# Kernel optimization log

Hardware: AMD Instinct MI355X
Metric: run time of the kernel (lower is better)

## Reference

```python
import jax, jax.numpy as jnp
import numpy as np
from jax import lax

P = 128   # patch_size
S = 64    # stride
K = 31    # PSF kernel size
NZ = 15   # number of Zernike coefficients
HID = 64  # aberration MLP hidden width


def setup_inputs() -> dict:
    key = jax.random.key(0)
    ks = jax.random.split(key, 8)
    B, C, H, W = 8, 3, 512, 512
    x_hat = jax.random.uniform(ks[0], (B, C, H, W), dtype=jnp.float32)
    w1 = jax.random.normal(ks[1], (2, HID), dtype=jnp.float32) * 0.5
    b1 = jnp.zeros((HID,), jnp.float32)
    w2 = jax.random.normal(ks[2], (HID, HID), dtype=jnp.float32) * 0.125
    b2 = jnp.zeros((HID,), jnp.float32)
    w3 = jax.random.normal(ks[3], (HID, NZ), dtype=jnp.float32) * 0.1
    b3 = jnp.zeros((NZ,), jnp.float32)
    zernike_basis = jax.random.normal(ks[4], (NZ, K, K), dtype=jnp.float32) * 0.5
    return {"x_hat": x_hat, "w1": w1, "b1": b1, "w2": w2, "b2": b2,
            "w3": w3, "b3": b3, "zernike_basis": zernike_basis}


def _hann(n):
    # torch.hann_window (periodic=True): 0.5*(1 - cos(2*pi*k/n))
    return 0.5 - 0.5 * jnp.cos(2.0 * jnp.pi * jnp.arange(n, dtype=jnp.float32) / n)


def _psf_from_coeffs(coeffs, basis):
    # coeffs: [N, NZ], basis: [NZ, K, K] -> normalized PSFs [N, K, K]
    phase = jnp.einsum('nz,zhw->nhw', coeffs, basis)          # [N, K, K]
    g = jnp.linspace(-1.0, 1.0, K, dtype=jnp.float32)
    r2 = g[:, None] ** 2 + g[None, :] ** 2
    mask = (r2 <= 1.0).astype(jnp.float32)                    # circular pupil
    pupil = mask * jnp.exp(1j * phase.astype(jnp.complex64))
    field = jnp.fft.fftshift(jnp.fft.fft2(jnp.fft.ifftshift(pupil, axes=(-2, -1))), axes=(-2, -1))
    psf = jnp.abs(field) ** 2
    psf = psf / (jnp.sum(psf, axis=(-2, -1), keepdims=True) + 1e-12)
    return psf


def _forward(x_hat, w1, b1, w2, b2, w3, b3, basis):
    B, C, H, W = x_hat.shape
    pad_h = (S - (H - P) % S) % S
    pad_w = (S - (W - P) % S) % S
    x = jnp.pad(x_hat, ((0, 0), (0, 0), (0, pad_h), (0, pad_w)), mode='reflect') \
        if (pad_h or pad_w) else x_hat
    H_pad, W_pad = x.shape[2], x.shape[3]
    n_h = (H_pad - P) // S + 1
    n_w = (W_pad - P) // S + 1
    N = n_h * n_w

    # ---- unfold into overlapping patches: [B*N, C, P, P] ----
    r0 = jnp.arange(n_h) * S
    c0 = jnp.arange(n_w) * S
    ridx = r0[:, None] + jnp.arange(P)[None, :]               # [n_h, P]
    cidx = c0[:, None] + jnp.arange(P)[None, :]               # [n_w, P]
    patches = x[:, :, ridx[:, None, :, None], cidx[None, :, None, :]]  # [B,C,n_h,n_w,P,P]
    patches = patches.transpose(0, 2, 3, 1, 4, 5).reshape(B * N, C, P, P)

    # ---- per-patch normalized center coords in [-1, 1] ----
    y_norm = (r0.astype(jnp.float32) + P / 2.0) / H_pad * 2.0 - 1.0
    x_norm = (c0.astype(jnp.float32) + P / 2.0) / W_pad * 2.0 - 1.0
    gy, gx = jnp.meshgrid(y_norm, x_norm, indexing='ij')
    coords = jnp.stack([gy, gx], axis=-1).reshape(N, 2)       # [N, 2]
    coords = jnp.tile(coords, (B, 1))                         # [B*N, 2]

    # ---- aberration MLP -> Zernike coeffs -> PSF kernels ----
    h = jax.nn.relu(coords @ w1 + b1)
    h = jax.nn.relu(h @ w2 + b2)
    coeffs = h @ w3 + b3                                      # [B*N, NZ]
    psf = _psf_from_coeffs(coeffs, basis)                     # [B*N, K, K], C_k = 1
    kf = psf[:, ::-1, ::-1]                                   # flip -> true convolution

    # ---- spatially varying per-patch conv (C>1, C_k==1 broadcast branch) ----
    BN = B * N
    pad = K // 2
    xp = jnp.pad(patches, ((0, 0), (0, 0), (pad, pad), (pad, pad)))
    lhs = xp.reshape(1, BN * C, P + 2 * pad, P + 2 * pad)
    rhs = jnp.broadcast_to(kf[:, None, :, :], (BN, C, K, K)).reshape(BN * C, 1, K, K)
    y = lax.conv_general_dilated(lhs, rhs, (1, 1), 'VALID',
                                 dimension_numbers=('NCHW', 'OIHW', 'NCHW'),
                                 feature_group_count=BN * C)
    y_patches = y.reshape(BN, C, P, P)

    # ---- Hann window + overlap-add fold ----
    hann = _hann(P)
    window = hann[:, None] * hann[None, :]                    # [P, P]
    y_patches = y_patches * window[None, None]

    idx = (ridx[:, None, :, None] * W_pad + cidx[None, :, None, :]).reshape(-1)  # [N*P*P]
    vals = y_patches.reshape(B, N, C, P, P).transpose(0, 2, 1, 3, 4).reshape(B, C, -1)
    y_accum = jnp.zeros((B, C, H_pad * W_pad), jnp.float32).at[:, :, idx].add(vals)
    y_accum = y_accum.reshape(B, C, H_pad, W_pad)

    wvals = jnp.broadcast_to(window, (N, P, P)).reshape(-1)
    w_accum = jnp.zeros((H_pad * W_pad,), jnp.float32).at[idx].add(wvals)
    w_accum = w_accum.reshape(1, 1, H_pad, W_pad)

    y_hat = y_accum / (w_accum + 1e-8)
    return y_hat[:, :, :H, :W]


def reference(x_hat, w1, b1, w2, b2, w3, b3, zernike_basis):
    return _forward(x_hat, w1, b1, w2, b2, w3, b3, zernike_basis)
```

## Files before the change

kernel.cpp:

```cpp
#include <hip/hip_runtime.h>
#include <math.h>

#define B_ 8
#define C_ 3
#define HW_ 512
#define P_ 128
#define S_ 64
#define K_ 31
#define NZ_ 15
#define HID_ 64
#define NPOS_ 49
#define BN_ (B_*NPOS_)

#define LSTRIDE_ 192
#define LROWB_ 384
#define TROWS_ 96
#define FRAG_U32_ 256
#define NSTEP_ 16
#define BPOS_U32_ (NSTEP_ * 3 * FRAG_U32_)

typedef __attribute__((ext_vector_type(8))) short bf16x8;
typedef __attribute__((ext_vector_type(4))) float f32x4;

__device__ __forceinline__ float hann128(int p) {
    return 0.5f - 0.5f * cosf(6.283185307179586f * (float)p / 128.0f);
}

__device__ __forceinline__ unsigned int bf16_rne(float f) {
    union { float f; unsigned int u; } v; v.f = f;
    unsigned int r = v.u + 0x7fffu + ((v.u >> 16) & 1u);
    return r >> 16;
}

__device__ __forceinline__ float bf16_to_f(unsigned int bits16) {
    union { unsigned int u; float f; } v; v.u = bits16 << 16;
    return v.f;
}

__global__ __launch_bounds__(1024) void psf_kernel(
    const float* __restrict__ w1, const float* __restrict__ b1,
    const float* __restrict__ w2, const float* __restrict__ b2,
    const float* __restrict__ w3, const float* __restrict__ b3,
    const float* __restrict__ basis, unsigned int* __restrict__ bfrags)
{
    __shared__ float h1[HID_], h2[HID_], coef[NZ_];
    __shared__ float pupR[961], pupI[961], tR[961], tI[961];
    __shared__ float rootR[31], rootI[31];
    __shared__ float red[16];
    int n = blockIdx.x;
    int nh = n / 7, nw = n % 7;
    int tid = threadIdx.x;
    float cy = (float)(nh * S_ + P_ / 2) * (2.0f / (float)HW_) - 1.0f;
    float cx = (float)(nw * S_ + P_ / 2) * (2.0f / (float)HW_) - 1.0f;

    if (tid < HID_) h1[tid] = fmaxf(0.0f, cy * w1[tid] + cx * w1[HID_ + tid] + b1[tid]);
    if (tid < 31) {
        float ang = -6.283185307179586f * (float)tid / 31.0f;
        rootR[tid] = cosf(ang);
        rootI[tid] = sinf(ang);
    }
    __syncthreads();
    if (tid < HID_) {
        float s = b2[tid];
        for (int k = 0; k < HID_; ++k) s = fmaf(h1[k], w2[k * HID_ + tid], s);
        h2[tid] = fmaxf(0.0f, s);
    }
    __syncthreads();
    if (tid < NZ_) {
        float s = b3[tid];
        for (int k = 0; k < HID_; ++k) s = fmaf(h2[k], w3[k * NZ_ + tid], s);
        coef[tid] = s;
    }
    __syncthreads();

    for (int idx = tid; idx < 961; idx += 1024) {
        int h = idx / 31, w = idx % 31;
        float ph = 0.0f;
        for (int z = 0; z < NZ_; ++z) ph = fmaf(coef[z], basis[z * 961 + idx], ph);
        int dh = h - 15, dw = w - 15;
        bool m = (dh * dh + dw * dw) <= 225;
        float sv, cv;
        sincosf(ph, &sv, &cv);
        pupR[idx] = m ? cv : 0.0f;
        pupI[idx] = m ? sv : 0.0f;
    }
    __syncthreads();

    for (int idx = tid; idx < 961; idx += 1024) {
        int h = idx / 31, k = idx % 31;
        float ar = 0.0f, ai = 0.0f;
        for (int w = 0; w < 31; ++w) {
            int tt = (k * w) % 31;
            float cr = rootR[tt], ci = rootI[tt];
            float pr = pupR[h * 31 + w], pi = pupI[h * 31 + w];
            ar += pr * cr - pi * ci;
            ai += pr * ci + pi * cr;
        }
        tR[idx] = ar; tI[idx] = ai;
    }
    __syncthreads();

    float lsum = 0.0f;
    for (int idx = tid; idx < 961; idx += 1024) {
        int u = idx / 31, k = idx % 31;
        float gr = 0.0f, gi = 0.0f;
        for (int h = 0; h < 31; ++h) {
            int tt = (u * h) % 31;
            float cr = rootR[tt], ci = rootI[tt];
            float ar = tR[h * 31 + k], ai = tI[h * 31 + k];
            gr += ar * cr - ai * ci;
            gi += ar * ci + ai * cr;
        }
        float p = gr * gr + gi * gi;
        pupR[idx] = p;
        lsum += p;
    }
    float v = lsum;
    #pragma unroll
    for (int off = 32; off >= 1; off >>= 1) v += __shfl_xor(v, off, 64);
    if ((tid & 63) == 0) red[tid >> 6] = v;
    __syncthreads();
    if (tid == 0) {
        float s = 0.0f;
        #pragma unroll
        for (int i = 0; i < 16; ++i) s += red[i];
        red[0] = 1.0f / (s + 1e-12f);
    }
    __syncthreads();
    float inv = red[0];
    for (int idx = tid; idx < 961; idx += 1024) {
        int j = idx / 31, i = idx % 31;
        int u = (15 - j + 31) % 31, vv = (15 - i + 31) % 31;
        tI[idx] = pupR[u * 31 + vv] * inv;
    }
    __syncthreads();

    unsigned int* bf = bfrags + (size_t)n * BPOS_U32_;
    for (int w2 = tid; w2 < BPOS_U32_; w2 += 1024) {
        int jc = w2 >> 8;
        int s = jc / 3, c = jc % 3;
        int rem = w2 & 255;
        int l = rem >> 2, ew = rem & 3;
        int nn = l & 15, kg = l >> 4;
        unsigned int pack = 0;
        #pragma unroll
        for (int q = 0; q < 2; ++q) {
            int e = ew * 2 + q;
            int kk = kg * 8 + e;
            int jrow = 2 * s + (kk >> 4);
            int tap = 16 * c + (kk & 15) - nn;
            float vx = (jrow >= 1 && jrow <= 31 && tap >= 1 && tap <= 31)
                       ? tI[(jrow - 1) * 31 + (tap - 1)] : 0.0f;
            pack |= bf16_rne(vx) << (16 * q);
        }
        bf[w2] = pack;
    }
}

template<int MODE>
__global__ __launch_bounds__(512, 4) void conv_mfma_kernel(
    const float* __restrict__ x, const unsigned int* __restrict__ bfrags,
    void* __restrict__ dst)
{
    __shared__ unsigned short sIn[TROWS_ * LSTRIDE_];
    __shared__ float sH[128];

    int t = blockIdx.x;
    int half = t & 1;
    int cc = (t >> 1) % 3;
    int bn = t / 6;
    int b = bn / NPOS_, n = bn % NPOS_;
    int nh = n / 7, nw = n % 7;
    int r0 = nh * S_, c0 = nw * S_;
    int tid = threadIdx.x;

    if (tid < 128) sH[tid] = hann128(tid);

    for (int i = tid; i < TROWS_ * LROWB_ / 16; i += 512)
        ((uint4*)sIn)[i] = make_uint4(0u, 0u, 0u, 0u);
    __syncthreads();

    const float* xb = x + ((size_t)(b * C_ + cc) * HW_ + r0) * HW_ + c0;
    int rpbase = half * 64 - 16;
    for (int i = tid; i < TROWS_ * 16; i += 512) {
        int r = i >> 4, c8 = (i & 15) * 8;
        int rp = rpbase + r;
        if (rp >= 0 && rp < P_) {
            float4 v0 = *(const float4*)&xb[rp * HW_ + c8];
            float4 v1 = *(const float4*)&xb[rp * HW_ + c8 + 4];
            uint4 o;
            o.x = bf16_rne(v0.x) | (bf16_rne(v0.y) << 16);
            o.y = bf16_rne(v0.z) | (bf16_rne(v0.w) << 16);
            o.z = bf16_rne(v1.x) | (bf16_rne(v1.y) << 16);
            o.w = bf16_rne(v1.z) | (bf16_rne(v1.w) << 16);
            int byteoff = (r * LROWB_ + 32 + c8 * 2) ^ ((r & 7) << 4);
            *(uint4*)((char*)sIn + byteoff) = o;
        }
    }
    __syncthreads();

    int lane = tid & 63, wv = tid >> 6;
    int m0 = (wv & 3) * 16;
    int ch = (wv >> 2) * 64;
    int lrow = lane & 15, lkg = lane >> 4;

    f32x4 acc[4];
    #pragma unroll
    for (int q = 0; q < 4; ++q) acc[q] = (f32x4){0.f, 0.f, 0.f, 0.f};

    int rowb = m0 + lrow + (lkg >> 1);
    int colb = ch * 2 + (lkg & 1) * 16;
    int xr[4];
    #pragma unroll
    for (int sm = 0; sm < 4; ++sm) xr[sm] = ((rowb + 2 * sm) & 7) << 4;
    const bf16x8* bpos = (const bf16x8*)(bfrags + (size_t)n * BPOS_U32_) + lane;

    bf16x8 A0[6], A1[6], B0[3], B1[3];

#define LOADA(DST, S) { int base_ = (rowb + 2 * (S)) * LROWB_ + colb; int x_ = xr[(S) & 3]; \
    _Pragma("unroll") for (int p_ = 0; p_ < 6; ++p_) \
        DST[p_] = *(const bf16x8*)((const char*)sIn + ((base_ + p_ * 32) ^ x_)); }
#define LOADB(DST, S) { const bf16x8* bp_ = bpos + (S) * 192; \
    DST[0] = bp_[0]; DST[1] = bp_[64]; DST[2] = bp_[128]; }
#define DOMFMA(AA, BB) { _Pragma("unroll") for (int q_ = 0; q_ < 4; ++q_) { \
    acc[q_] = __builtin_amdgcn_mfma_f32_16x16x32_bf16(AA[q_],     BB[0], acc[q_], 0, 0, 0); \
    acc[q_] = __builtin_amdgcn_mfma_f32_16x16x32_bf16(AA[q_ + 1], BB[1], acc[q_], 0, 0, 0); \
    acc[q_] = __builtin_amdgcn_mfma_f32_16x16x32_bf16(AA[q_ + 2], BB[2], acc[q_], 0, 0, 0); } }

    LOADA(A0, 0); LOADB(B0, 0);

    #pragma unroll
    for (int s2 = 0; s2 < 8; ++s2) {
        LOADA(A1, 2 * s2 + 1); LOADB(B1, 2 * s2 + 1);
        __builtin_amdgcn_sched_barrier(0);
        __builtin_amdgcn_s_setprio(1);
        DOMFMA(A0, B0);
        __builtin_amdgcn_s_setprio(0);
        __builtin_amdgcn_sched_barrier(0);
        if (s2 < 7) { LOADA(A0, 2 * s2 + 2); LOADB(B0, 2 * s2 + 2); }
        __builtin_amdgcn_sched_barrier(0);
        __builtin_amdgcn_s_setprio(1);
        DOMFMA(A1, B1);
        __builtin_amdgcn_s_setprio(0);
        __builtin_amdgcn_sched_barrier(0);
    }
#undef LOADA
#undef LOADB
#undef DOMFMA

    int prow0 = half * 64 + m0 + lkg * 4;
    float hy[4];
    #pragma unroll
    for (int r = 0; r < 4; ++r) hy[r] = sH[prow0 + r];

    #pragma unroll
    for (int q = 0; q < 4; ++q) {
        int pcol = ch + 16 * q + lrow;
        float hxv = sH[pcol];
        #pragma unroll
        for (int r = 0; r < 4; ++r) {
            int prow = prow0 + r;
            float val = acc[q][r] * hy[r] * hxv;
            if (MODE == 0) {
                unsigned short* yp = (unsigned short*)dst + (((size_t)bn * C_ + cc) << 14);
                yp[prow * P_ + pcol] = (unsigned short)bf16_rne(val);
            } else {
                float* ob = (float*)dst;
                atomicAdd(ob + ((size_t)(b * C_ + cc) * HW_ + r0 + prow) * HW_ + c0 + pcol, val);
            }
        }
    }
}

__global__ __launch_bounds__(256) void gather_kernel(
    const unsigned short* __restrict__ ypatch, float* __restrict__ out)
{
    __shared__ float sH[128];
    int tid = threadIdx.x;
    if (tid < 128) sH[tid] = hann128(tid);
    __syncthreads();

    int gid = blockIdx.x * 256 + tid;
    int base = gid * 4;
    if (base >= B_ * C_ * HW_ * HW_) return;
    int X = base & 511;
    int Y = (base >> 9) & 511;
    int bc = base >> 18;
    int c = bc % 3, b = bc / 3;
    int nhA = Y >> 6, pyA = Y & 63;
    int nwA = X >> 6, pxA = X & 63;
    bool vA = nhA <= 6, vB = nhA >= 1;
    bool uA = nwA <= 6, uB = nwA >= 1;
    float wy = (vA ? sH[pyA] : 0.0f) + (vB ? sH[pyA + 64] : 0.0f);

    float4 acc = {0.f, 0.f, 0.f, 0.f};
    #pragma unroll
    for (int sy = 0; sy < 2; ++sy) {
        bool okY = sy == 0 ? vA : vB;
        int nh = sy == 0 ? nhA : nhA - 1;
        int py = sy == 0 ? pyA : pyA + 64;
        #pragma unroll
        for (int sx = 0; sx < 2; ++sx) {
            bool okX = sx == 0 ? uA : uB;
            int nw = sx == 0 ? nwA : nwA - 1;
            int px = sx == 0 ? pxA : pxA + 64;
            if (okY && okX) {
                size_t off = ((((size_t)b * NPOS_ + nh * 7 + nw) * C_ + c) << 14) + (py << 7) + px;
                uint2 v = *(const uint2*)&ypatch[off];
                acc.x += bf16_to_f(v.x & 0xffffu);
                acc.y += bf16_to_f(v.x >> 16);
                acc.z += bf16_to_f(v.y & 0xffffu);
                acc.w += bf16_to_f(v.y >> 16);
            }
        }
    }
    float4 o;
    float wx0 = (uA ? sH[pxA + 0] : 0.0f) + (uB ? sH[pxA + 64] : 0.0f);
    float wx1 = (uA ? sH[pxA + 1] : 0.0f) + (uB ? sH[pxA + 65] : 0.0f);
    float wx2 = (uA ? sH[pxA + 2] : 0.0f) + (uB ? sH[pxA + 66] : 0.0f);
    float wx3 = (uA ? sH[pxA + 3] : 0.0f) + (uB ? sH[pxA + 67] : 0.0f);
    o.x = acc.x / (wy * wx0 + 1e-8f);
    o.y = acc.y / (wy * wx1 + 1e-8f);
    o.z = acc.z / (wy * wx2 + 1e-8f);
    o.w = acc.w / (wy * wx3 + 1e-8f);
    *(float4*)&out[base] = o;
}

__global__ __launch_bounds__(256) void divide_kernel(float* __restrict__ out)
{
    int idx = blockIdx.x * 256 + threadIdx.x;
    if (idx >= B_ * C_ * HW_ * HW_) return;
    int X = idx & 511;
    int Y = (idx >> 9) & 511;
    int nhA = Y >> 6, pyA = Y & 63;
    int nwA = X >> 6, pxA = X & 63;
    float wy = (nhA <= 6 ? hann128(pyA) : 0.0f) + (nhA >= 1 ? hann128(pyA + 64) : 0.0f);
    float wx = (nwA <= 6 ? hann128(pxA) : 0.0f) + (nwA >= 1 ? hann128(pxA + 64) : 0.0f);
    out[idx] = out[idx] / (wy * wx + 1e-8f);
}

extern "C" void kernel_launch(void* const* d_in, const int* in_sizes, int n_in,
                              void* d_out, int out_size, void* d_ws, size_t ws_size,
                              hipStream_t stream)
{
    const float* x    = (const float*)d_in[0];
    const float* w1   = (const float*)d_in[1];
    const float* b1   = (const float*)d_in[2];
    const float* w2   = (const float*)d_in[3];
    const float* b2   = (const float*)d_in[4];
    const float* w3   = (const float*)d_in[5];
    const float* b3   = (const float*)d_in[6];
    const float* basis = (const float*)d_in[7];
    float* out = (float*)d_out;

    unsigned int* bfrags = (unsigned int*)d_ws;
    size_t bfBytes = (size_t)NPOS_ * BPOS_U32_ * sizeof(unsigned int);
    size_t need = bfBytes + (size_t)BN_ * C_ * P_ * P_ * sizeof(unsigned short);

    psf_kernel<<<NPOS_, 1024, 0, stream>>>(w1, b1, w2, b2, w3, b3, basis, bfrags);

    int nPix = B_ * C_ * HW_ * HW_;
    if (ws_size >= need) {
        unsigned short* ypatch = (unsigned short*)((char*)d_ws + bfBytes);
        conv_mfma_kernel<0><<<BN_ * C_ * 2, 512, 0, stream>>>(x, bfrags, ypatch);
        gather_kernel<<<(nPix / 4 + 255) / 256, 256, 0, stream>>>(ypatch, out);
    } else {
        hipMemsetAsync(d_out, 0, (size_t)out_size * sizeof(float), stream);
        conv_mfma_kernel<1><<<BN_ * C_ * 2, 512, 0, stream>>>(x, bfrags, out);
        divide_kernel<<<(nPix + 255) / 256, 256, 0, stream>>>(out);
    }
}
```

Baseline: 80.83 us.

## Process full patch per block with 16x128 wave tiles and staggered step order

Each block now handles a whole 128x128 patch instead of half, so the input tile is loaded once into a 160-row LDS buffer rather than twice with halo overlap. Each wave computes a 16x128 output strip (8 accumulators), which lets A fragments be reused across more columns. Each wave also starts its K-step loop at a different offset, which spreads out LDS and global B-fragment accesses. The explicit double-buffered A pipeline with sched barriers is replaced by single-buffered A loads plus B prefetch. In exchange the grid is halved, LDS use rises, and register pressure grows from the larger accumulator and A arrays, which may reduce occupancy and latency hiding.

```diff
diff --git a/kernel.cpp b/kernel.cpp
--- a/kernel.cpp
+++ b/kernel.cpp
@@ -12,9 +12,8 @@
 #define NPOS_ 49
 #define BN_ (B_*NPOS_)
 
-#define LSTRIDE_ 192
 #define LROWB_ 384
-#define TROWS_ 96
+#define TROWS_ 160
 #define FRAG_U32_ 256
 #define NSTEP_ 16
 #define BPOS_U32_ (NSTEP_ * 3 * FRAG_U32_)
@@ -162,13 +161,12 @@
     const float* __restrict__ x, const unsigned int* __restrict__ bfrags,
     void* __restrict__ dst)
 {
-    __shared__ unsigned short sIn[TROWS_ * LSTRIDE_];
+    __shared__ unsigned short sIn[TROWS_ * (LROWB_ / 2)];
     __shared__ float sH[128];
 
     int t = blockIdx.x;
-    int half = t & 1;
-    int cc = (t >> 1) % 3;
-    int bn = t / 6;
+    int cc = t % 3;
+    int bn = t / 3;
     int b = bn / NPOS_, n = bn % NPOS_;
     int nh = n / 7, nw = n % 7;
     int r0 = nh * S_, c0 = nw * S_;
@@ -181,81 +179,74 @@
     __syncthreads();
 
     const float* xb = x + ((size_t)(b * C_ + cc) * HW_ + r0) * HW_ + c0;
-    int rpbase = half * 64 - 16;
-    for (int i = tid; i < TROWS_ * 16; i += 512) {
-        int r = i >> 4, c8 = (i & 15) * 8;
-        int rp = rpbase + r;
-        if (rp >= 0 && rp < P_) {
-            float4 v0 = *(const float4*)&xb[rp * HW_ + c8];
-            float4 v1 = *(const float4*)&xb[rp * HW_ + c8 + 4];
-            uint4 o;
-            o.x = bf16_rne(v0.x) | (bf16_rne(v0.y) << 16);
-            o.y = bf16_rne(v0.z) | (bf16_rne(v0.w) << 16);
-            o.z = bf16_rne(v1.x) | (bf16_rne(v1.y) << 16);
-            o.w = bf16_rne(v1.z) | (bf16_rne(v1.w) << 16);
-            int byteoff = (r * LROWB_ + 32 + c8 * 2) ^ ((r & 7) << 4);
-            *(uint4*)((char*)sIn + byteoff) = o;
-        }
+    for (int i = tid; i < 128 * 16; i += 512) {
+        int r = 16 + (i >> 4), c8 = (i & 15) * 8;
+        const float* rp = &xb[(r - 16) * HW_ + c8];
+        float4 v0 = *(const float4*)rp;
+        float4 v1 = *(const float4*)(rp + 4);
+        uint4 o;
+        o.x = bf16_rne(v0.x) | (bf16_rne(v0.y) << 16);
+        o.y = bf16_rne(v0.z) | (bf16_rne(v0.w) << 16);
+        o.z = bf16_rne(v1.x) | (bf16_rne(v1.y) << 16);
+        o.w = bf16_rne(v1.z) | (bf16_rne(v1.w) << 16);
+        int byteoff = (r * LROWB_ + 32 + c8 * 2) ^ ((r & 7) << 4);
+        *(uint4*)((char*)sIn + byteoff) = o;
     }
     __syncthreads();
 
     int lane = tid & 63, wv = tid >> 6;
-    int m0 = (wv & 3) * 16;
-    int ch = (wv >> 2) * 64;
+    int m0 = wv * 16;
     int lrow = lane & 15, lkg = lane >> 4;
 
-    f32x4 acc[4];
-    #pragma unroll
-    for (int q = 0; q < 4; ++q) acc[q] = (f32x4){0.f, 0.f, 0.f, 0.f};
+    f32x4 acc[8];
+    #pragma unroll
+    for (int q = 0; q < 8; ++q) acc[q] = (f32x4){0.f, 0.f, 0.f, 0.f};
 
     int rowb = m0 + lrow + (lkg >> 1);
-    int colb = ch * 2 + (lkg & 1) * 16;
-    int xr[4];
-    #pragma unroll
-    for (int sm = 0; sm < 4; ++sm) xr[sm] = ((rowb + 2 * sm) & 7) << 4;
+    int colb = (lkg & 1) * 16;
     const bf16x8* bpos = (const bf16x8*)(bfrags + (size_t)n * BPOS_U32_) + lane;
-
-    bf16x8 A0[6], A1[6], B0[3], B1[3];
-
-#define LOADA(DST, S) { int base_ = (rowb + 2 * (S)) * LROWB_ + colb; int x_ = xr[(S) & 3]; \
-    _Pragma("unroll") for (int p_ = 0; p_ < 6; ++p_) \
-        DST[p_] = *(const bf16x8*)((const char*)sIn + ((base_ + p_ * 32) ^ x_)); }
-#define LOADB(DST, S) { const bf16x8* bp_ = bpos + (S) * 192; \
-    DST[0] = bp_[0]; DST[1] = bp_[64]; DST[2] = bp_[128]; }
-#define DOMFMA(AA, BB) { _Pragma("unroll") for (int q_ = 0; q_ < 4; ++q_) { \
-    acc[q_] = __builtin_amdgcn_mfma_f32_16x16x32_bf16(AA[q_],     BB[0], acc[q_], 0, 0, 0); \
-    acc[q_] = __builtin_amdgcn_mfma_f32_16x16x32_bf16(AA[q_ + 1], BB[1], acc[q_], 0, 0, 0); \
-    acc[q_] = __builtin_amdgcn_mfma_f32_16x16x32_bf16(AA[q_ + 2], BB[2], acc[q_], 0, 0, 0); } }
-
-    LOADA(A0, 0); LOADB(B0, 0);
-
-    #pragma unroll
-    for (int s2 = 0; s2 < 8; ++s2) {
-        LOADA(A1, 2 * s2 + 1); LOADB(B1, 2 * s2 + 1);
-        __builtin_amdgcn_sched_barrier(0);
+    int sbase = wv * 2;
+
+    int ss0 = sbase & 15;
+    bf16x8 Bc0 = bpos[ss0 * 192], Bc1 = bpos[ss0 * 192 + 64], Bc2 = bpos[ss0 * 192 + 128];
+
+    #pragma unroll 2
+    for (int s = 0; s < NSTEP_; ++s) {
+        int ss = (s + sbase) & 15;
+        bf16x8 Bn0, Bn1, Bn2;
+        if (s + 1 < NSTEP_) {
+            int ssn = (s + 1 + sbase) & 15;
+            const bf16x8* bp = bpos + ssn * 192;
+            Bn0 = bp[0]; Bn1 = bp[64]; Bn2 = bp[128];
+        } else { Bn0 = Bc0; Bn1 = Bc1; Bn2 = Bc2; }
+
+        int r2 = rowb + 2 * ss;
+        int base = r2 * LROWB_ + colb;
+        int xorv = (r2 & 7) << 4;
+        bf16x8 A[10];
+        #pragma unroll
+        for (int p = 0; p < 10; ++p)
+            A[p] = *(const bf16x8*)((const char*)sIn + ((base + p * 32) ^ xorv));
+
         __builtin_amdgcn_s_setprio(1);
-        DOMFMA(A0, B0);
+        #pragma unroll
+        for (int q = 0; q < 8; ++q) {
+            acc[q] = __builtin_amdgcn_mfma_f32_16x16x32_bf16(A[q],     Bc0, acc[q], 0, 0, 0);
+            acc[q] = __builtin_amdgcn_mfma_f32_16x16x32_bf16(A[q + 1], Bc1, acc[q], 0, 0, 0);
+            acc[q] = __builtin_amdgcn_mfma_f32_16x16x32_bf16(A[q + 2], Bc2, acc[q], 0, 0, 0);
+        }
         __builtin_amdgcn_s_setprio(0);
-        __builtin_amdgcn_sched_barrier(0);
-        if (s2 < 7) { LOADA(A0, 2 * s2 + 2); LOADB(B0, 2 * s2 + 2); }
-        __builtin_amdgcn_sched_barrier(0);
-        __builtin_amdgcn_s_setprio(1);
-        DOMFMA(A1, B1);
-        __builtin_amdgcn_s_setprio(0);
-        __builtin_amdgcn_sched_barrier(0);
-    }
-#undef LOADA
-#undef LOADB
-#undef DOMFMA
-
-    int prow0 = half * 64 + m0 + lkg * 4;
+        Bc0 = Bn0; Bc1 = Bn1; Bc2 = Bn2;
+    }
+
+    int prow0 = m0 + lkg * 4;
     float hy[4];
     #pragma unroll
     for (int r = 0; r < 4; ++r) hy[r] = sH[prow0 + r];
 
     #pragma unroll
-    for (int q = 0; q < 4; ++q) {
-        int pcol = ch + 16 * q + lrow;
+    for (int q = 0; q < 8; ++q) {
+        int pcol = 16 * q + lrow;
         float hxv = sH[pcol];
         #pragma unroll
         for (int r = 0; r < 4; ++r) {
@@ -362,11 +353,11 @@
     int nPix = B_ * C_ * HW_ * HW_;
     if (ws_size >= need) {
         unsigned short* ypatch = (unsigned short*)((char*)d_ws + bfBytes);
-        conv_mfma_kernel<0><<<BN_ * C_ * 2, 512, 0, stream>>>(x, bfrags, ypatch);
+        conv_mfma_kernel<0><<<BN_ * C_, 512, 0, stream>>>(x, bfrags, ypatch);
         gather_kernel<<<(nPix / 4 + 255) / 256, 256, 0, stream>>>(ypatch, out);
     } else {
         hipMemsetAsync(d_out, 0, (size_t)out_size * sizeof(float), stream);
-        conv_mfma_kernel<1><<<BN_ * C_ * 2, 512, 0, stream>>>(x, bfrags, out);
+        conv_mfma_kernel<1><<<BN_ * C_, 512, 0, stream>>>(x, bfrags, out);
         divide_kernel<<<(nPix + 255) / 256, 256, 0, stream>>>(out);
     }
 }
```

Result: faster. 77.52 us (-4.1%).

## Widen per-wave conv tile to full 128 columns with inline-asm pipelined loads

Applied to the files above, without the earlier changes.

The conv block shrinks from 512 to 256 threads, and each wave now computes a 16x128 output strip with 8 accumulators instead of 16x64. A fragments loaded from LDS are then reused across twice as many MFMAs, and each B fragment is loaded once per wave instead of by two waves. LDS and global loads are issued through inline asm with explicit partial waitcnts, and each wave starts at a staggered k-step to spread bank and cache traffic. The cost is more registers per thread, a lower occupancy hint, and manual waitcnt counting that must match the number of loads in flight.

```diff
diff --git a/kernel.cpp b/kernel.cpp
--- a/kernel.cpp
+++ b/kernel.cpp
@@ -12,7 +12,6 @@
 #define NPOS_ 49
 #define BN_ (B_*NPOS_)
 
-#define LSTRIDE_ 192
 #define LROWB_ 384
 #define TROWS_ 96
 #define FRAG_U32_ 256
@@ -158,11 +157,11 @@
 }
 
 template<int MODE>
-__global__ __launch_bounds__(512, 4) void conv_mfma_kernel(
+__global__ __launch_bounds__(256, 3) void conv_mfma_kernel(
     const float* __restrict__ x, const unsigned int* __restrict__ bfrags,
     void* __restrict__ dst)
 {
-    __shared__ unsigned short sIn[TROWS_ * LSTRIDE_];
+    __shared__ unsigned short sIn[TROWS_ * (LROWB_ / 2)];
     __shared__ float sH[128];
 
     int t = blockIdx.x;
@@ -176,13 +175,13 @@
 
     if (tid < 128) sH[tid] = hann128(tid);
 
-    for (int i = tid; i < TROWS_ * LROWB_ / 16; i += 512)
+    for (int i = tid; i < TROWS_ * LROWB_ / 16; i += 256)
         ((uint4*)sIn)[i] = make_uint4(0u, 0u, 0u, 0u);
     __syncthreads();
 
     const float* xb = x + ((size_t)(b * C_ + cc) * HW_ + r0) * HW_ + c0;
     int rpbase = half * 64 - 16;
-    for (int i = tid; i < TROWS_ * 16; i += 512) {
+    for (int i = tid; i < TROWS_ * 16; i += 256) {
         int r = i >> 4, c8 = (i & 15) * 8;
         int rp = rpbase + r;
         if (rp >= 0 && rp < P_) {
@@ -200,52 +199,72 @@
     __syncthreads();
 
     int lane = tid & 63, wv = tid >> 6;
-    int m0 = (wv & 3) * 16;
-    int ch = (wv >> 2) * 64;
+    int m0 = wv * 16;
     int lrow = lane & 15, lkg = lane >> 4;
 
-    f32x4 acc[4];
-    #pragma unroll
-    for (int q = 0; q < 4; ++q) acc[q] = (f32x4){0.f, 0.f, 0.f, 0.f};
+    f32x4 acc[8];
+    #pragma unroll
+    for (int q = 0; q < 8; ++q) acc[q] = (f32x4){0.f, 0.f, 0.f, 0.f};
 
     int rowb = m0 + lrow + (lkg >> 1);
-    int colb = ch * 2 + (lkg & 1) * 16;
-    int xr[4];
-    #pragma unroll
-    for (int sm = 0; sm < 4; ++sm) xr[sm] = ((rowb + 2 * sm) & 7) << 4;
+    int colb = (lkg & 1) * 16;
+    unsigned lbase = (unsigned)(unsigned long long)(const void*)sIn;
     const bf16x8* bpos = (const bf16x8*)(bfrags + (size_t)n * BPOS_U32_) + lane;
-
-    bf16x8 A0[6], A1[6], B0[3], B1[3];
-
-#define LOADA(DST, S) { int base_ = (rowb + 2 * (S)) * LROWB_ + colb; int x_ = xr[(S) & 3]; \
-    _Pragma("unroll") for (int p_ = 0; p_ < 6; ++p_) \
-        DST[p_] = *(const bf16x8*)((const char*)sIn + ((base_ + p_ * 32) ^ x_)); }
-#define LOADB(DST, S) { const bf16x8* bp_ = bpos + (S) * 192; \
-    DST[0] = bp_[0]; DST[1] = bp_[64]; DST[2] = bp_[128]; }
-#define DOMFMA(AA, BB) { _Pragma("unroll") for (int q_ = 0; q_ < 4; ++q_) { \
+    int sbase = wv * 4;
+
+    bf16x8 A0[10], A1[10], B0[3], B1[3];
+
+#define ISSUE_A(DST, SS_) { \
+    int r2_ = rowb + 2 * (SS_); \
+    unsigned ro_ = (unsigned)(r2_ * LROWB_ + colb); \
+    unsigned xv_ = (unsigned)((r2_ & 7) << 4); \
+    _Pragma("unroll") \
+    for (int p_ = 0; p_ < 10; ++p_) { \
+        unsigned a_ = lbase + ((ro_ + (unsigned)(p_ * 32)) ^ xv_); \
+        asm volatile("ds_read_b128 %0, %1" : "=v"(DST[p_]) : "v"(a_)); \
+    } }
+
+#define ISSUE_B(DST, SS_) { \
+    const char* bp_ = (const char*)(bpos + (SS_) * 192); \
+    asm volatile("global_load_dwordx4 %0, %1, off"             : "=v"(DST[0]) : "v"(bp_)); \
+    asm volatile("global_load_dwordx4 %0, %1, off offset:1024" : "=v"(DST[1]) : "v"(bp_)); \
+    asm volatile("global_load_dwordx4 %0, %1, off offset:2048" : "=v"(DST[2]) : "v"(bp_)); }
+
+#define DOMFMA(AA, BB) { _Pragma("unroll") for (int q_ = 0; q_ < 8; ++q_) { \
     acc[q_] = __builtin_amdgcn_mfma_f32_16x16x32_bf16(AA[q_],     BB[0], acc[q_], 0, 0, 0); \
     acc[q_] = __builtin_amdgcn_mfma_f32_16x16x32_bf16(AA[q_ + 1], BB[1], acc[q_], 0, 0, 0); \
     acc[q_] = __builtin_amdgcn_mfma_f32_16x16x32_bf16(AA[q_ + 2], BB[2], acc[q_], 0, 0, 0); } }
 
-    LOADA(A0, 0); LOADB(B0, 0);
+    {
+        int ss0 = sbase & 15;
+        ISSUE_A(A0, ss0); ISSUE_B(B0, ss0);
+    }
 
     #pragma unroll
     for (int s2 = 0; s2 < 8; ++s2) {
-        LOADA(A1, 2 * s2 + 1); LOADB(B1, 2 * s2 + 1);
+        int se = (2 * s2 + 1 + sbase) & 15;
+        ISSUE_A(A1, se); ISSUE_B(B1, se);
+        asm volatile("s_waitcnt lgkmcnt(10) vmcnt(3)");
         __builtin_amdgcn_sched_barrier(0);
         __builtin_amdgcn_s_setprio(1);
         DOMFMA(A0, B0);
         __builtin_amdgcn_s_setprio(0);
         __builtin_amdgcn_sched_barrier(0);
-        if (s2 < 7) { LOADA(A0, 2 * s2 + 2); LOADB(B0, 2 * s2 + 2); }
+        if (s2 < 7) {
+            int so = (2 * s2 + 2 + sbase) & 15;
+            ISSUE_A(A0, so); ISSUE_B(B0, so);
+            asm volatile("s_waitcnt lgkmcnt(10) vmcnt(3)");
+        } else {
+            asm volatile("s_waitcnt lgkmcnt(0) vmcnt(0)");
+        }
         __builtin_amdgcn_sched_barrier(0);
         __builtin_amdgcn_s_setprio(1);
         DOMFMA(A1, B1);
         __builtin_amdgcn_s_setprio(0);
         __builtin_amdgcn_sched_barrier(0);
     }
-#undef LOADA
-#undef LOADB
+#undef ISSUE_A
+#undef ISSUE_B
 #undef DOMFMA
 
     int prow0 = half * 64 + m0 + lkg * 4;
@@ -254,8 +273,8 @@
     for (int r = 0; r < 4; ++r) hy[r] = sH[prow0 + r];
 
     #pragma unroll
-    for (int q = 0; q < 4; ++q) {
-        int pcol = ch + 16 * q + lrow;
+    for (int q = 0; q < 8; ++q) {
+        int pcol = 16 * q + lrow;
         float hxv = sH[pcol];
         #pragma unroll
         for (int r = 0; r < 4; ++r) {
@@ -362,11 +381,11 @@
     int nPix = B_ * C_ * HW_ * HW_;
     if (ws_size >= need) {
         unsigned short* ypatch = (unsigned short*)((char*)d_ws + bfBytes);
-        conv_mfma_kernel<0><<<BN_ * C_ * 2, 512, 0, stream>>>(x, bfrags, ypatch);
+        conv_mfma_kernel<0><<<BN_ * C_ * 2, 256, 0, stream>>>(x, bfrags, ypatch);
         gather_kernel<<<(nPix / 4 + 255) / 256, 256, 0, stream>>>(ypatch, out);
     } else {
         hipMemsetAsync(d_out, 0, (size_t)out_size * sizeof(float), stream);
-        conv_mfma_kernel<1><<<BN_ * C_ * 2, 512, 0, stream>>>(x, bfrags, out);
+        conv_mfma_kernel<1><<<BN_ * C_ * 2, 256, 0, stream>>>(x, bfrags, out);
         divide_kernel<<<(nPix + 255) / 256, 256, 0, stream>>>(out);
     }
 }
```

Result: faster. 79.05 us (-2.2%).
